# Kernel optimization log

Measured on AMD Instinct MI355X. Metric: run time of the kernel, lower is better.

The kernel has to match this reference:

```python
import jax, jax.numpy as jnp
import numpy as np

K = 512          # num_embeddings
D = 64           # embedding_dim
BETA = 0.25      # commitment_cost
DECAY = 0.99
EPS = 1e-5


def setup_inputs() -> dict:
    key = jax.random.key(0)
    k1, k2, k3 = jax.random.split(key, 3)
    inputs = jax.random.normal(k1, (64, D, 32, 32), dtype=jnp.float32)  # NCHW, C == embedding_dim
    embedding = jax.random.normal(k2, (K, D), dtype=jnp.float32)
    ema_w = jax.random.normal(k3, (K, D), dtype=jnp.float32)
    ema_cluster_size = jnp.zeros((K,), dtype=jnp.float32)
    return {"inputs": inputs, "embedding": embedding, "ema_w": ema_w,
            "ema_cluster_size": ema_cluster_size}


def reference(inputs, embedding, ema_w, ema_cluster_size):
    # NCHW -> NHWC, flatten to [N, D]
    x = jnp.transpose(inputs, (0, 2, 3, 1))
    B, H, W, C = x.shape
    flat = x.reshape(-1, C)                                   # [N, D]

    # squared L2 distances to all codes: [N, K]
    d = (jnp.sum(flat * flat, axis=1, keepdims=True)
         + jnp.sum(embedding * embedding, axis=1)
         - 2.0 * flat @ embedding.T)
    idx = jnp.argmin(d, axis=1)                               # [N]

    # gather (equivalent to one-hot @ embedding, without materializing one-hot)
    quantized = embedding[idx].reshape(x.shape)               # [B,H,W,D]

    # EMA codebook update (training branch); segment sums replace encodings.T matmuls
    counts = jax.ops.segment_sum(jnp.ones_like(idx, dtype=flat.dtype), idx,
                                 num_segments=K)              # [K]
    new_cs = ema_cluster_size * DECAY + (1.0 - DECAY) * counts
    n = jnp.sum(new_cs)
    new_cs = (new_cs + EPS) / (n + K * EPS) * n               # Laplace smoothing
    dw = jax.ops.segment_sum(flat, idx, num_segments=K)       # [K, D]
    new_ema_w = ema_w * DECAY + (1.0 - DECAY) * dw
    new_embedding = new_ema_w / new_cs[:, None]

    # commitment loss + straight-through estimator
    e_latent_loss = jnp.mean((jax.lax.stop_gradient(quantized) - x) ** 2)
    loss = BETA * e_latent_loss
    quantized_st = x + jax.lax.stop_gradient(quantized - x)

    avg_probs = counts / flat.shape[0]
    perplexity = jnp.exp(-jnp.sum(avg_probs * jnp.log(avg_probs + 1e-10)))

    out_q = jnp.transpose(quantized_st, (0, 3, 1, 2))         # back to NCHW
    return (loss, out_q, perplexity, idx.reshape(B, H, W),
            new_cs, new_ema_w, new_embedding)
```

## Files before the change

kernel.cpp:

```cpp
#include <hip/hip_runtime.h>

#define K_CODES 512
#define DIM 64
#define HW 1024
#define NVEC 65536
#define NREP 8

#define O0 0
#define O1 1
#define O2 4194305
#define O3 4194306
#define O4 4259842
#define O5 4260354
#define O6 4293122

#define WS_EE   0
#define WS_CNT  512
#define WS_LOSS 4608
#define WS_N    6656
#define WS_DW   6912
#define WS_BP   269056

typedef __bf16 bf16x8 __attribute__((ext_vector_type(8)));
typedef float  f32x4  __attribute__((ext_vector_type(4)));

union U2 { unsigned int u; unsigned short us[2]; __bf16 h[2]; };

__global__ void k0_init(const float* __restrict__ emb, const float* __restrict__ ema_cs,
                        float* __restrict__ wsf) {
    __shared__ float sn[256];
    const int b = blockIdx.x, t = threadIdx.x;
    if (b < 128) {
        #pragma unroll
        for (int i = 0; i < 8; ++i)
            wsf[WS_DW + b * 2048 + i * 256 + t] = 0.0f;
    } else if (b == 128) {
        int* cnt = (int*)(wsf + WS_CNT);
        #pragma unroll
        for (int i = 0; i < 16; ++i) cnt[i * 256 + t] = 0;
        sn[t] = ema_cs[t] + ema_cs[t + 256];
        __syncthreads();
        for (int s = 128; s > 0; s >>= 1) {
            if (t < s) sn[t] += sn[t + s];
            __syncthreads();
        }
        if (t == 0) wsf[WS_N] = 0.99f * sn[0] + 0.01f * 65536.0f;
    } else if (b < 131) {
        int k = (b - 129) * 256 + t;
        const float* e = emb + k * DIM;
        float s = 0.0f;
        #pragma unroll
        for (int c = 0; c < DIM; ++c) s += e[c] * e[c];
        wsf[WS_EE + k] = s;
    } else {
        int g = (b - 131) * 256 + t;
        int j    = g & 7;
        int lane = (g >> 3) & 63;
        int ks   = (g >> 9) & 1;
        int rest = g >> 10;
        int ntg  = rest & 31;
        int s    = rest >> 5;
        int code = ntg * 16 + (lane & 15);
        int c    = ks * 32 + (lane >> 4) * 8 + j;
        float v = -2.0f * emb[code * DIM + c];
        __bf16 h0 = (__bf16)v;  float r1 = v  - (float)h0;
        __bf16 h1 = (__bf16)r1; float r2 = r1 - (float)h1;
        __bf16 hv = (s == 0) ? h0 : (s == 1 ? h1 : (__bf16)r2);
        ((__bf16*)(wsf + WS_BP))[g] = hv;
    }
}

__global__ __launch_bounds__(256, 4)
void k1_main(const float* __restrict__ in, const float* __restrict__ emb,
             float* __restrict__ out, float* __restrict__ wsf) {
    __shared__ unsigned int xsp[3][32 * 36];
    __shared__ float xxp[32][9];
    __shared__ float pmin[4][32];
    __shared__ int   pidx[4][32];
    __shared__ float xxs[32];
    __shared__ int   hist[K_CODES];

    const int t    = threadIdx.x;
    const int lane = t & 63;
    const int wave = t >> 6;
    const int ni   = wave;
    const int col  = lane & 15;
    const int quad = lane >> 4;

    hist[t] = 0; hist[t + 256] = 0;

    const int blk     = blockIdx.x;
    const int rep     = blk & (NREP - 1);
    const int n_img   = blk >> 5;
    const int hw_base = (blk & 31) * 32;
    const float* xbase = in + n_img * (DIM * HW) + hw_base;

    f32x4 acc[2][8];
    #pragma unroll
    for (int nt = 0; nt < 8; ++nt) {
        float eev = wsf[WS_EE + ni * 128 + nt * 16 + col];
        #pragma unroll
        for (int mi = 0; mi < 2; ++mi) {
            acc[mi][nt][0] = eev; acc[mi][nt][1] = eev;
            acc[mi][nt][2] = eev; acc[mi][nt][3] = eev;
        }
    }

    {
        const int h   = t & 31;
        const int cp0 = t >> 5;
        float xxa = 0.0f;
        #pragma unroll
        for (int it = 0; it < 4; ++it) {
            int cp = it * 8 + cp0;
            float v0 = xbase[(2 * cp) * HW + h];
            float v1 = xbase[(2 * cp + 1) * HW + h];
            __bf16 a0 = (__bf16)v0; float ra = v0 - (float)a0;
            __bf16 a1 = (__bf16)ra; ra -= (float)a1;
            __bf16 a2 = (__bf16)ra;
            __bf16 b0 = (__bf16)v1; float rb = v1 - (float)b0;
            __bf16 b1 = (__bf16)rb; rb -= (float)b1;
            __bf16 b2 = (__bf16)rb;
            U2 u0, u1, u2;
            u0.h[0] = a0; u0.h[1] = b0;
            u1.h[0] = a1; u1.h[1] = b1;
            u2.h[0] = a2; u2.h[1] = b2;
            xsp[0][h * 36 + cp] = u0.u;
            xsp[1][h * 36 + cp] = u1.u;
            xsp[2][h * 36 + cp] = u2.u;
            xxa += v0 * v0 + v1 * v1;
        }
        xxp[h][cp0] = xxa;
    }

    const bf16x8* bp8 = (const bf16x8*)(wsf + WS_BP);

    bf16x8 Bp[3][4];
    #pragma unroll
    for (int n4 = 0; n4 < 4; ++n4)
        Bp[0][n4] = bp8[(((0 * 32 + ni * 8 + 0 * 4 + n4) * 2 + 0) * 64) + lane];
    #pragma unroll
    for (int n4 = 0; n4 < 4; ++n4)
        Bp[1][n4] = bp8[(((0 * 32 + ni * 8 + 1 * 4 + n4) * 2 + 0) * 64) + lane];

    __syncthreads();

    if (t < 32) {
        float s = 0.0f;
        #pragma unroll
        for (int j = 0; j < 8; ++j) s += xxp[t][j];
        xxs[t] = s;
    }

    bf16x8 Af[2][3][2];
    #pragma unroll
    for (int ks = 0; ks < 2; ++ks)
        #pragma unroll
        for (int mi = 0; mi < 2; ++mi) {
            int u = (mi * 16 + col) * 36 + ks * 16 + quad * 4;
            Af[ks][0][mi] = *(const bf16x8*)&xsp[0][u];
            Af[ks][1][mi] = *(const bf16x8*)&xsp[1][u];
            Af[ks][2][mi] = *(const bf16x8*)&xsp[2][u];
        }

    #pragma unroll
    for (int p = 0; p < 12; ++p) {
        const int ks = p / 6, s = (p % 6) / 2, bh = p & 1;
        if (p < 10) {
            const int pn = p + 2;
            const int ksn = pn / 6, sn = (pn % 6) / 2, bhn = pn & 1;
            #pragma unroll
            for (int n4 = 0; n4 < 4; ++n4)
                Bp[pn % 3][n4] = bp8[(((sn * 32 + ni * 8 + bhn * 4 + n4) * 2 + ksn) * 64) + lane];
        }
        #pragma unroll
        for (int mi = 0; mi < 2; ++mi)
            #pragma unroll
            for (int n4 = 0; n4 < 4; ++n4)
                acc[mi][bh * 4 + n4] = __builtin_amdgcn_mfma_f32_16x16x32_bf16(
                    Af[ks][0][mi], Bp[p % 3][n4], acc[mi][bh * 4 + n4], 0, 0, 0);
        if (s < 2) {
            #pragma unroll
            for (int mi = 0; mi < 2; ++mi)
                #pragma unroll
                for (int n4 = 0; n4 < 4; ++n4)
                    acc[mi][bh * 4 + n4] = __builtin_amdgcn_mfma_f32_16x16x32_bf16(
                        Af[ks][1][mi], Bp[p % 3][n4], acc[mi][bh * 4 + n4], 0, 0, 0);
        }
        if (s == 0) {
            #pragma unroll
            for (int mi = 0; mi < 2; ++mi)
                #pragma unroll
                for (int n4 = 0; n4 < 4; ++n4)
                    acc[mi][bh * 4 + n4] = __builtin_amdgcn_mfma_f32_16x16x32_bf16(
                        Af[ks][2][mi], Bp[p % 3][n4], acc[mi][bh * 4 + n4], 0, 0, 0);
        }
    }

    #pragma unroll
    for (int mi = 0; mi < 2; ++mi) {
        #pragma unroll
        for (int r = 0; r < 4; ++r) {
            float v  = acc[mi][0][r];
            int   bi = ni * 128 + col;
            #pragma unroll
            for (int nt = 1; nt < 8; ++nt) {
                float u  = acc[mi][nt][r];
                int   ui = ni * 128 + nt * 16 + col;
                if (u < v) { v = u; bi = ui; }
            }
            #pragma unroll
            for (int off = 1; off < 16; off <<= 1) {
                float ov = __shfl_xor(v, off);
                int   oi = __shfl_xor(bi, off);
                if (ov < v || (ov == v && oi < bi)) { v = ov; bi = oi; }
            }
            if (col == 0) {
                int row = mi * 16 + quad * 4 + r;
                pmin[ni][row] = v;
                pidx[ni][row] = bi;
            }
        }
    }
    __syncthreads();

    if (t < 32) {
        float v = pmin[0][t]; int bi = pidx[0][t];
        #pragma unroll
        for (int q = 1; q < 4; ++q) {
            float u = pmin[q][t]; int ui = pidx[q][t];
            if (u < v) { v = u; bi = ui; }
        }
        pidx[0][t] = bi;
        out[O3 + blk * 32 + t] = (float)bi;
        atomicAdd(&hist[bi], 1);
        float ld = v + xxs[t];
        #pragma unroll
        for (int off = 16; off > 0; off >>= 1) ld += __shfl_down(ld, off);
        if (t == 0) wsf[WS_LOSS + blk] = ld;
    }
    __syncthreads();

    {
        int v = t & 31, cq = t >> 5;
        int kv = pidx[0][v];
        const float* ew = emb + kv * DIM;
        float* oq = out + O1 + n_img * (DIM * HW) + hw_base + v;
        #pragma unroll
        for (int c = cq * 8; c < cq * 8 + 8; ++c) oq[c * HW] = ew[c];
    }

    {
        float* dwr = wsf + WS_DW + rep * 32768;
        #pragma unroll
        for (int v8 = 0; v8 < 8; ++v8) {
            int v  = wave * 8 + v8;
            int kv = pidx[0][v];
            int wi = v * 36 + (lane >> 1);
            U2 a0, a1, a2;
            a0.u = xsp[0][wi]; a1.u = xsp[1][wi]; a2.u = xsp[2][wi];
            int hs = lane & 1;
            float val = (float)a0.h[hs] + (float)a1.h[hs] + (float)a2.h[hs];
            atomicAdd(&dwr[kv * 64 + lane], val);
        }
    }

    int* cnt = (int*)(wsf + WS_CNT);
    if (hist[t])       atomicAdd(&cnt[rep * 512 + t], hist[t]);
    if (hist[t + 256]) atomicAdd(&cnt[rep * 512 + t + 256], hist[t + 256]);
}

__global__ void k2(const float* __restrict__ ema_cs, const float* __restrict__ ema_w,
                   float* __restrict__ out, const float* __restrict__ wsf) {
    __shared__ float s1[256], s2[256];
    const int t = threadIdx.x;
    const int blk = blockIdx.x;
    const int* cnt = (const int*)(wsf + WS_CNT);

    if (blk == 128) {
        float ls = 0.0f;
        #pragma unroll
        for (int j = 0; j < 8; ++j) ls += wsf[WS_LOSS + j * 256 + t];
        s1[t] = ls;
        float ca = 0.0f, cb = 0.0f;
        #pragma unroll
        for (int r = 0; r < NREP; ++r) {
            ca += (float)cnt[r * 512 + t];
            cb += (float)cnt[r * 512 + 256 + t];
        }
        float pa = ca * (1.0f / 65536.0f);
        float pb = cb * (1.0f / 65536.0f);
        s2[t] = pa * logf(pa + 1e-10f) + pb * logf(pb + 1e-10f);
        __syncthreads();
        for (int s = 128; s > 0; s >>= 1) {
            if (t < s) { s1[t] += s1[t + s]; s2[t] += s2[t + s]; }
            __syncthreads();
        }
        if (t == 0) {
            out[O0] = 0.25f * s1[0] * (1.0f / 4194304.0f);
            out[O2] = expf(-s2[0]);
        }
        return;
    }

    const int m = blk * 256 + t;
    const int k = m >> 6;
    float ck = 0.0f, dwsum = 0.0f;
    #pragma unroll
    for (int r = 0; r < NREP; ++r) {
        ck    += (float)cnt[r * 512 + k];
        dwsum += wsf[WS_DW + r * 32768 + m];
    }
    float n    = wsf[WS_N];
    float rawk = 0.99f * ema_cs[k] + 0.01f * ck;
    float csk  = (rawk + 1e-5f) / (n + 512.0f * 1e-5f) * n;
    float wv   = 0.99f * ema_w[m] + 0.01f * dwsum;
    out[O5 + m] = wv;
    out[O6 + m] = wv / csk;
    if ((m & 63) == 0) out[O4 + k] = csk;
}

extern "C" void kernel_launch(void* const* d_in, const int* in_sizes, int n_in,
                              void* d_out, int out_size, void* d_ws, size_t ws_size,
                              hipStream_t stream) {
    const float* in     = (const float*)d_in[0];
    const float* emb    = (const float*)d_in[1];
    const float* ema_w  = (const float*)d_in[2];
    const float* ema_cs = (const float*)d_in[3];
    float* out = (float*)d_out;
    float* wsf = (float*)d_ws;

    hipLaunchKernelGGL(k0_init, dim3(515),  dim3(256), 0, stream, emb, ema_cs, wsf);
    hipLaunchKernelGGL(k1_main, dim3(2048), dim3(256), 0, stream, in, emb, out, wsf);
    hipLaunchKernelGGL(k2,      dim3(129),  dim3(256), 0, stream, ema_cs, ema_w, out, wsf);
}
```

Baseline: 138.7 us.

## Process two tiles per block with input prefetch and widen accumulator replicas

Each block of the main kernel now handles two 32-vector tiles. The second tile's input loads are issued into registers before the first tile's MFMA work, then split into bf16 parts after it, so global load latency overlaps compute. The grid is halved to 1024 blocks, shared split buffers are double-buffered, and the block-local histogram is reset between tiles. Separately, dw/count replicas grow from 8 to 32 to spread atomic contention, which costs larger workspace zeroing in the init kernel and more reduction work in the finalize kernel.

```diff
diff --git a/kernel.cpp b/kernel.cpp
--- a/kernel.cpp
+++ b/kernel.cpp
@@ -4,7 +4,7 @@
 #define DIM 64
 #define HW 1024
 #define NVEC 65536
-#define NREP 8
+#define NREP 32
 
 #define O0 0
 #define O1 1
@@ -16,10 +16,10 @@
 
 #define WS_EE   0
 #define WS_CNT  512
-#define WS_LOSS 4608
-#define WS_N    6656
-#define WS_DW   6912
-#define WS_BP   269056
+#define WS_LOSS 16896
+#define WS_N    18944
+#define WS_DW   19200
+#define WS_BP   1067776
 
 typedef __bf16 bf16x8 __attribute__((ext_vector_type(8)));
 typedef float  f32x4  __attribute__((ext_vector_type(4)));
@@ -30,14 +30,14 @@
                         float* __restrict__ wsf) {
     __shared__ float sn[256];
     const int b = blockIdx.x, t = threadIdx.x;
-    if (b < 128) {
+    if (b < 512) {
         #pragma unroll
         for (int i = 0; i < 8; ++i)
             wsf[WS_DW + b * 2048 + i * 256 + t] = 0.0f;
-    } else if (b == 128) {
+    } else if (b == 512) {
         int* cnt = (int*)(wsf + WS_CNT);
         #pragma unroll
-        for (int i = 0; i < 16; ++i) cnt[i * 256 + t] = 0;
+        for (int i = 0; i < 64; ++i) cnt[i * 256 + t] = 0;
         sn[t] = ema_cs[t] + ema_cs[t + 256];
         __syncthreads();
         for (int s = 128; s > 0; s >>= 1) {
@@ -45,15 +45,15 @@
             __syncthreads();
         }
         if (t == 0) wsf[WS_N] = 0.99f * sn[0] + 0.01f * 65536.0f;
-    } else if (b < 131) {
-        int k = (b - 129) * 256 + t;
+    } else if (b < 515) {
+        int k = (b - 513) * 256 + t;
         const float* e = emb + k * DIM;
         float s = 0.0f;
         #pragma unroll
         for (int c = 0; c < DIM; ++c) s += e[c] * e[c];
         wsf[WS_EE + k] = s;
     } else {
-        int g = (b - 131) * 256 + t;
+        int g = (b - 515) * 256 + t;
         int j    = g & 7;
         int lane = (g >> 3) & 63;
         int ks   = (g >> 9) & 1;
@@ -70,11 +70,36 @@
     }
 }
 
+#define BUILD_SPLITS(SV, BUF)                                                  \
+    {                                                                          \
+        float xxa = 0.0f;                                                      \
+        _Pragma("unroll")                                                      \
+        for (int it = 0; it < 4; ++it) {                                       \
+            int cp = it * 8 + cp0;                                             \
+            float v0 = SV[2 * it], v1 = SV[2 * it + 1];                        \
+            __bf16 a0 = (__bf16)v0; float ra = v0 - (float)a0;                 \
+            __bf16 a1 = (__bf16)ra; ra -= (float)a1;                           \
+            __bf16 a2 = (__bf16)ra;                                            \
+            __bf16 b0 = (__bf16)v1; float rb = v1 - (float)b0;                 \
+            __bf16 b1 = (__bf16)rb; rb -= (float)b1;                           \
+            __bf16 b2 = (__bf16)rb;                                            \
+            U2 u0, u1, u2;                                                     \
+            u0.h[0] = a0; u0.h[1] = b0;                                        \
+            u1.h[0] = a1; u1.h[1] = b1;                                        \
+            u2.h[0] = a2; u2.h[1] = b2;                                        \
+            xsp[BUF][0][h * 36 + cp] = u0.u;                                   \
+            xsp[BUF][1][h * 36 + cp] = u1.u;                                   \
+            xsp[BUF][2][h * 36 + cp] = u2.u;                                   \
+            xxa += v0 * v0 + v1 * v1;                                          \
+        }                                                                      \
+        xxp[BUF][h][cp0] = xxa;                                                \
+    }
+
 __global__ __launch_bounds__(256, 4)
 void k1_main(const float* __restrict__ in, const float* __restrict__ emb,
              float* __restrict__ out, float* __restrict__ wsf) {
-    __shared__ unsigned int xsp[3][32 * 36];
-    __shared__ float xxp[32][9];
+    __shared__ unsigned int xsp[2][3][32 * 36];
+    __shared__ float xxp[2][32][9];
     __shared__ float pmin[4][32];
     __shared__ int   pidx[4][32];
     __shared__ float xxs[32];
@@ -86,188 +111,196 @@
     const int ni   = wave;
     const int col  = lane & 15;
     const int quad = lane >> 4;
+    const int h    = t & 31;
+    const int cp0  = t >> 5;
 
     hist[t] = 0; hist[t + 256] = 0;
 
-    const int blk     = blockIdx.x;
-    const int rep     = blk & (NREP - 1);
-    const int n_img   = blk >> 5;
-    const int hw_base = (blk & 31) * 32;
-    const float* xbase = in + n_img * (DIM * HW) + hw_base;
-
-    f32x4 acc[2][8];
-    #pragma unroll
-    for (int nt = 0; nt < 8; ++nt) {
-        float eev = wsf[WS_EE + ni * 128 + nt * 16 + col];
-        #pragma unroll
-        for (int mi = 0; mi < 2; ++mi) {
-            acc[mi][nt][0] = eev; acc[mi][nt][1] = eev;
-            acc[mi][nt][2] = eev; acc[mi][nt][3] = eev;
-        }
-    }
+    const int blk = blockIdx.x;
+    const int rep = blk & (NREP - 1);
 
     {
-        const int h   = t & 31;
-        const int cp0 = t >> 5;
-        float xxa = 0.0f;
+        const int g0 = blk * 2;
+        const float* xb = in + (g0 >> 5) * (DIM * HW) + (g0 & 31) * 32;
+        float sv[8];
         #pragma unroll
         for (int it = 0; it < 4; ++it) {
             int cp = it * 8 + cp0;
-            float v0 = xbase[(2 * cp) * HW + h];
-            float v1 = xbase[(2 * cp + 1) * HW + h];
-            __bf16 a0 = (__bf16)v0; float ra = v0 - (float)a0;
-            __bf16 a1 = (__bf16)ra; ra -= (float)a1;
-            __bf16 a2 = (__bf16)ra;
-            __bf16 b0 = (__bf16)v1; float rb = v1 - (float)b0;
-            __bf16 b1 = (__bf16)rb; rb -= (float)b1;
-            __bf16 b2 = (__bf16)rb;
-            U2 u0, u1, u2;
-            u0.h[0] = a0; u0.h[1] = b0;
-            u1.h[0] = a1; u1.h[1] = b1;
-            u2.h[0] = a2; u2.h[1] = b2;
-            xsp[0][h * 36 + cp] = u0.u;
-            xsp[1][h * 36 + cp] = u1.u;
-            xsp[2][h * 36 + cp] = u2.u;
-            xxa += v0 * v0 + v1 * v1;
-        }
-        xxp[h][cp0] = xxa;
-    }
+            sv[2 * it]     = xb[(2 * cp) * HW + h];
+            sv[2 * it + 1] = xb[(2 * cp + 1) * HW + h];
+        }
+        BUILD_SPLITS(sv, 0)
+    }
+
+    float sv1[8];
+    {
+        const int g1 = blk * 2 + 1;
+        const float* xb = in + (g1 >> 5) * (DIM * HW) + (g1 & 31) * 32;
+        #pragma unroll
+        for (int it = 0; it < 4; ++it) {
+            int cp = it * 8 + cp0;
+            sv1[2 * it]     = xb[(2 * cp) * HW + h];
+            sv1[2 * it + 1] = xb[(2 * cp + 1) * HW + h];
+        }
+    }
+    __syncthreads();
 
     const bf16x8* bp8 = (const bf16x8*)(wsf + WS_BP);
 
-    bf16x8 Bp[3][4];
-    #pragma unroll
-    for (int n4 = 0; n4 < 4; ++n4)
-        Bp[0][n4] = bp8[(((0 * 32 + ni * 8 + 0 * 4 + n4) * 2 + 0) * 64) + lane];
-    #pragma unroll
-    for (int n4 = 0; n4 < 4; ++n4)
-        Bp[1][n4] = bp8[(((0 * 32 + ni * 8 + 1 * 4 + n4) * 2 + 0) * 64) + lane];
-
-    __syncthreads();
-
-    if (t < 32) {
-        float s = 0.0f;
-        #pragma unroll
-        for (int j = 0; j < 8; ++j) s += xxp[t][j];
-        xxs[t] = s;
-    }
-
-    bf16x8 Af[2][3][2];
-    #pragma unroll
-    for (int ks = 0; ks < 2; ++ks)
-        #pragma unroll
-        for (int mi = 0; mi < 2; ++mi) {
-            int u = (mi * 16 + col) * 36 + ks * 16 + quad * 4;
-            Af[ks][0][mi] = *(const bf16x8*)&xsp[0][u];
-            Af[ks][1][mi] = *(const bf16x8*)&xsp[1][u];
-            Af[ks][2][mi] = *(const bf16x8*)&xsp[2][u];
-        }
-
-    #pragma unroll
-    for (int p = 0; p < 12; ++p) {
-        const int ks = p / 6, s = (p % 6) / 2, bh = p & 1;
-        if (p < 10) {
-            const int pn = p + 2;
-            const int ksn = pn / 6, sn = (pn % 6) / 2, bhn = pn & 1;
-            #pragma unroll
-            for (int n4 = 0; n4 < 4; ++n4)
-                Bp[pn % 3][n4] = bp8[(((sn * 32 + ni * 8 + bhn * 4 + n4) * 2 + ksn) * 64) + lane];
-        }
-        #pragma unroll
-        for (int mi = 0; mi < 2; ++mi)
-            #pragma unroll
-            for (int n4 = 0; n4 < 4; ++n4)
-                acc[mi][bh * 4 + n4] = __builtin_amdgcn_mfma_f32_16x16x32_bf16(
-                    Af[ks][0][mi], Bp[p % 3][n4], acc[mi][bh * 4 + n4], 0, 0, 0);
-        if (s < 2) {
+    #pragma unroll 1
+    for (int tl = 0; tl < 2; ++tl) {
+        const int gtile   = blk * 2 + tl;
+        const int n_img   = gtile >> 5;
+        const int hw_base = (gtile & 31) * 32;
+
+        f32x4 acc[2][8];
+        #pragma unroll
+        for (int nt = 0; nt < 8; ++nt) {
+            float eev = wsf[WS_EE + ni * 128 + nt * 16 + col];
+            #pragma unroll
+            for (int mi = 0; mi < 2; ++mi) {
+                acc[mi][nt][0] = eev; acc[mi][nt][1] = eev;
+                acc[mi][nt][2] = eev; acc[mi][nt][3] = eev;
+            }
+        }
+
+        if (t < 32) {
+            float s = 0.0f;
+            #pragma unroll
+            for (int j = 0; j < 8; ++j) s += xxp[tl][t][j];
+            xxs[t] = s;
+        }
+
+        bf16x8 Af[2][3][2];
+        #pragma unroll
+        for (int ks = 0; ks < 2; ++ks)
+            #pragma unroll
+            for (int mi = 0; mi < 2; ++mi) {
+                int u = (mi * 16 + col) * 36 + ks * 16 + quad * 4;
+                Af[ks][0][mi] = *(const bf16x8*)&xsp[tl][0][u];
+                Af[ks][1][mi] = *(const bf16x8*)&xsp[tl][1][u];
+                Af[ks][2][mi] = *(const bf16x8*)&xsp[tl][2][u];
+            }
+
+        bf16x8 Bp[3][4];
+        #pragma unroll
+        for (int n4 = 0; n4 < 4; ++n4)
+            Bp[0][n4] = bp8[(((ni * 8 + n4) * 2 + 0) * 64) + lane];
+        #pragma unroll
+        for (int n4 = 0; n4 < 4; ++n4)
+            Bp[1][n4] = bp8[(((ni * 8 + 4 + n4) * 2 + 0) * 64) + lane];
+
+        #pragma unroll
+        for (int p = 0; p < 12; ++p) {
+            const int ks = p / 6, s = (p % 6) / 2, bh = p & 1;
+            if (p < 10) {
+                const int pn = p + 2;
+                const int ksn = pn / 6, sn = (pn % 6) / 2, bhn = pn & 1;
+                #pragma unroll
+                for (int n4 = 0; n4 < 4; ++n4)
+                    Bp[pn % 3][n4] = bp8[(((sn * 32 + ni * 8 + bhn * 4 + n4) * 2 + ksn) * 64) + lane];
+            }
             #pragma unroll
             for (int mi = 0; mi < 2; ++mi)
                 #pragma unroll
                 for (int n4 = 0; n4 < 4; ++n4)
                     acc[mi][bh * 4 + n4] = __builtin_amdgcn_mfma_f32_16x16x32_bf16(
-                        Af[ks][1][mi], Bp[p % 3][n4], acc[mi][bh * 4 + n4], 0, 0, 0);
-        }
-        if (s == 0) {
-            #pragma unroll
-            for (int mi = 0; mi < 2; ++mi)
-                #pragma unroll
-                for (int n4 = 0; n4 < 4; ++n4)
-                    acc[mi][bh * 4 + n4] = __builtin_amdgcn_mfma_f32_16x16x32_bf16(
-                        Af[ks][2][mi], Bp[p % 3][n4], acc[mi][bh * 4 + n4], 0, 0, 0);
-        }
-    }
-
-    #pragma unroll
-    for (int mi = 0; mi < 2; ++mi) {
-        #pragma unroll
-        for (int r = 0; r < 4; ++r) {
-            float v  = acc[mi][0][r];
-            int   bi = ni * 128 + col;
-            #pragma unroll
-            for (int nt = 1; nt < 8; ++nt) {
-                float u  = acc[mi][nt][r];
-                int   ui = ni * 128 + nt * 16 + col;
+                        Af[ks][0][mi], Bp[p % 3][n4], acc[mi][bh * 4 + n4], 0, 0, 0);
+            if (s < 2) {
+                #pragma unroll
+                for (int mi = 0; mi < 2; ++mi)
+                    #pragma unroll
+                    for (int n4 = 0; n4 < 4; ++n4)
+                        acc[mi][bh * 4 + n4] = __builtin_amdgcn_mfma_f32_16x16x32_bf16(
+                            Af[ks][1][mi], Bp[p % 3][n4], acc[mi][bh * 4 + n4], 0, 0, 0);
+            }
+            if (s == 0) {
+                #pragma unroll
+                for (int mi = 0; mi < 2; ++mi)
+                    #pragma unroll
+                    for (int n4 = 0; n4 < 4; ++n4)
+                        acc[mi][bh * 4 + n4] = __builtin_amdgcn_mfma_f32_16x16x32_bf16(
+                            Af[ks][2][mi], Bp[p % 3][n4], acc[mi][bh * 4 + n4], 0, 0, 0);
+            }
+        }
+
+        #pragma unroll
+        for (int mi = 0; mi < 2; ++mi) {
+            #pragma unroll
+            for (int r = 0; r < 4; ++r) {
+                float v  = acc[mi][0][r];
+                int   bi = ni * 128 + col;
+                #pragma unroll
+                for (int nt = 1; nt < 8; ++nt) {
+                    float u  = acc[mi][nt][r];
+                    int   ui = ni * 128 + nt * 16 + col;
+                    if (u < v) { v = u; bi = ui; }
+                }
+                #pragma unroll
+                for (int off = 1; off < 16; off <<= 1) {
+                    float ov = __shfl_xor(v, off);
+                    int   oi = __shfl_xor(bi, off);
+                    if (ov < v || (ov == v && oi < bi)) { v = ov; bi = oi; }
+                }
+                if (col == 0) {
+                    int row = mi * 16 + quad * 4 + r;
+                    pmin[ni][row] = v;
+                    pidx[ni][row] = bi;
+                }
+            }
+        }
+        __syncthreads();
+
+        if (t < 32) {
+            float v = pmin[0][t]; int bi = pidx[0][t];
+            #pragma unroll
+            for (int q = 1; q < 4; ++q) {
+                float u = pmin[q][t]; int ui = pidx[q][t];
                 if (u < v) { v = u; bi = ui; }
             }
-            #pragma unroll
-            for (int off = 1; off < 16; off <<= 1) {
-                float ov = __shfl_xor(v, off);
-                int   oi = __shfl_xor(bi, off);
-                if (ov < v || (ov == v && oi < bi)) { v = ov; bi = oi; }
-            }
-            if (col == 0) {
-                int row = mi * 16 + quad * 4 + r;
-                pmin[ni][row] = v;
-                pidx[ni][row] = bi;
-            }
-        }
-    }
-    __syncthreads();
-
-    if (t < 32) {
-        float v = pmin[0][t]; int bi = pidx[0][t];
-        #pragma unroll
-        for (int q = 1; q < 4; ++q) {
-            float u = pmin[q][t]; int ui = pidx[q][t];
-            if (u < v) { v = u; bi = ui; }
-        }
-        pidx[0][t] = bi;
-        out[O3 + blk * 32 + t] = (float)bi;
-        atomicAdd(&hist[bi], 1);
-        float ld = v + xxs[t];
-        #pragma unroll
-        for (int off = 16; off > 0; off >>= 1) ld += __shfl_down(ld, off);
-        if (t == 0) wsf[WS_LOSS + blk] = ld;
-    }
-    __syncthreads();
-
-    {
-        int v = t & 31, cq = t >> 5;
-        int kv = pidx[0][v];
-        const float* ew = emb + kv * DIM;
-        float* oq = out + O1 + n_img * (DIM * HW) + hw_base + v;
-        #pragma unroll
-        for (int c = cq * 8; c < cq * 8 + 8; ++c) oq[c * HW] = ew[c];
-    }
-
-    {
-        float* dwr = wsf + WS_DW + rep * 32768;
-        #pragma unroll
-        for (int v8 = 0; v8 < 8; ++v8) {
-            int v  = wave * 8 + v8;
+            pidx[0][t] = bi;
+            out[O3 + gtile * 32 + t] = (float)bi;
+            atomicAdd(&hist[bi], 1);
+            float ld = v + xxs[t];
+            #pragma unroll
+            for (int off = 16; off > 0; off >>= 1) ld += __shfl_down(ld, off);
+            if (t == 0) wsf[WS_LOSS + gtile] = ld;
+        }
+        __syncthreads();
+
+        {
+            int v = t & 31, cq = t >> 5;
             int kv = pidx[0][v];
-            int wi = v * 36 + (lane >> 1);
-            U2 a0, a1, a2;
-            a0.u = xsp[0][wi]; a1.u = xsp[1][wi]; a2.u = xsp[2][wi];
-            int hs = lane & 1;
-            float val = (float)a0.h[hs] + (float)a1.h[hs] + (float)a2.h[hs];
-            atomicAdd(&dwr[kv * 64 + lane], val);
-        }
-    }
-
-    int* cnt = (int*)(wsf + WS_CNT);
-    if (hist[t])       atomicAdd(&cnt[rep * 512 + t], hist[t]);
-    if (hist[t + 256]) atomicAdd(&cnt[rep * 512 + t + 256], hist[t + 256]);
+            const float* ew = emb + kv * DIM;
+            float* oq = out + O1 + n_img * (DIM * HW) + hw_base + v;
+            #pragma unroll
+            for (int c = cq * 8; c < cq * 8 + 8; ++c) oq[c * HW] = ew[c];
+        }
+
+        {
+            float* dwr = wsf + WS_DW + rep * 32768;
+            #pragma unroll
+            for (int v8 = 0; v8 < 8; ++v8) {
+                int v  = wave * 8 + v8;
+                int kv = pidx[0][v];
+                int wi = v * 36 + (lane >> 1);
+                U2 a0, a1, a2;
+                a0.u = xsp[tl][0][wi]; a1.u = xsp[tl][1][wi]; a2.u = xsp[tl][2][wi];
+                int hs = lane & 1;
+                float val = (float)a0.h[hs] + (float)a1.h[hs] + (float)a2.h[hs];
+                atomicAdd(&dwr[kv * 64 + lane], val);
+            }
+        }
+
+        int* cnt = (int*)(wsf + WS_CNT);
+        if (hist[t])       { atomicAdd(&cnt[rep * 512 + t], hist[t]); hist[t] = 0; }
+        if (hist[t + 256]) { atomicAdd(&cnt[rep * 512 + t + 256], hist[t + 256]); hist[t + 256] = 0; }
+
+        if (tl == 0) {
+            BUILD_SPLITS(sv1, 1)
+            __syncthreads();
+        }
+    }
 }
 
 __global__ void k2(const float* __restrict__ ema_cs, const float* __restrict__ ema_w,
@@ -330,7 +363,7 @@
     float* out = (float*)d_out;
     float* wsf = (float*)d_ws;
 
-    hipLaunchKernelGGL(k0_init, dim3(515),  dim3(256), 0, stream, emb, ema_cs, wsf);
-    hipLaunchKernelGGL(k1_main, dim3(2048), dim3(256), 0, stream, in, emb, out, wsf);
+    hipLaunchKernelGGL(k0_init, dim3(899),  dim3(256), 0, stream, emb, ema_cs, wsf);
+    hipLaunchKernelGGL(k1_main, dim3(1024), dim3(256), 0, stream, in, emb, out, wsf);
     hipLaunchKernelGGL(k2,      dim3(129),  dim3(256), 0, stream, ema_cs, ema_w, out, wsf);
 }
```

Measured after the change: 218.0 us. 1.57x slower.
